# Kernel tuning notes

Measured on AMD Instinct MI355X. Metric: run time of the kernel, lower is better.

The kernel has to match this reference:

```python
import jax, jax.numpy as jnp
import numpy as np

N = 50000      # nodes
E = 600000     # edges
D_IN = 5
D_H = 128
EPS = 1e-5     # BatchNorm1d default eps


def batch_norm(x, gamma, beta):
    # training-mode BN over the node dimension (biased variance)
    m = jnp.mean(x, axis=0)
    v = jnp.var(x, axis=0)
    return (x - m) * jax.lax.rsqrt(v + EPS) * gamma + beta


def gcn_conv(x, W, b, src, dst, w):
    # PyG GCNConv: linear transform, add self-loops (weight 1),
    # symmetric normalization D^-1/2 A D^-1/2, scatter-add to dst, + bias.
    x = x @ W                                   # [N, out]
    n = x.shape[0]
    loop = jnp.arange(n)
    src = jnp.concatenate([src, loop])
    dst = jnp.concatenate([dst, loop])
    w = jnp.concatenate([w, jnp.ones((n,), w.dtype)])
    deg = jax.ops.segment_sum(w, dst, num_segments=n)
    dis = jnp.where(deg > 0, jax.lax.rsqrt(jnp.maximum(deg, 1e-12)), 0.0)
    norm = dis[src] * w * dis[dst]              # [E+N]
    msgs = norm[:, None] * x[src]               # gather + scale
    return jax.ops.segment_sum(msgs, dst, num_segments=n) + b


def setup_inputs() -> dict:
    key = jax.random.key(0)
    ks = jax.random.split(key, 20)
    s_in = 1.0 / np.sqrt(D_IN)
    s_h = 1.0 / np.sqrt(D_H)
    return {
        "h": jax.random.normal(ks[0], (N, D_IN), jnp.float32),
        "edge_index": jax.random.randint(ks[1], (2, E), 0, N),
        "edge_weight": jax.random.uniform(ks[2], (E,), jnp.float32),
        "g0": 1.0 + 0.1 * jax.random.normal(ks[3], (D_IN,), jnp.float32),
        "be0": 0.1 * jax.random.normal(ks[4], (D_IN,), jnp.float32),
        "W1": jax.random.normal(ks[5], (D_IN, D_H), jnp.float32) * s_in,
        "b1": jax.random.normal(ks[6], (D_H,), jnp.float32) * s_in,
        "g1": 1.0 + 0.1 * jax.random.normal(ks[7], (D_H,), jnp.float32),
        "be1": 0.1 * jax.random.normal(ks[8], (D_H,), jnp.float32),
        "W2": jax.random.normal(ks[9], (D_H, D_H), jnp.float32) * s_h,
        "b2": jax.random.normal(ks[10], (D_H,), jnp.float32) * s_h,
        "g2": 1.0 + 0.1 * jax.random.normal(ks[11], (D_H,), jnp.float32),
        "be2": 0.1 * jax.random.normal(ks[12], (D_H,), jnp.float32),
        "Wmu": jax.random.normal(ks[13], (D_H, D_H), jnp.float32) * s_h,
        "bmu": jax.random.normal(ks[14], (D_H,), jnp.float32) * s_h,
        "Wls": jax.random.normal(ks[15], (D_H, D_H), jnp.float32) * s_h,
        "bls": jax.random.normal(ks[16], (D_H,), jnp.float32) * s_h,
    }


def reference(h, edge_index, edge_weight, g0, be0, W1, b1, g1, be1,
              W2, b2, g2, be2, Wmu, bmu, Wls, bls):
    src, dst = edge_index[0], edge_index[1]
    h = batch_norm(h, g0, be0)
    h = jax.nn.relu(batch_norm(gcn_conv(h, W1, b1, src, dst, edge_weight), g1, be1))
    # dropout p=0.1 treated as eval-mode (identity)
    h = jax.nn.relu(batch_norm(gcn_conv(h, W2, b2, src, dst, edge_weight), g2, be2))
    mu = h @ Wmu + bmu
    log_std = h @ Wls + bls
    return (mu, log_std)
```

## Files before the change

### kernel.cpp

```cpp
#include <hip/hip_runtime.h>

#define N_NODES 50000
#define N_EDGES 600000
#define D_IN 5
#define D_H 128
#define BN_EPS 1e-5f
#define SCAN_BLOCKS ((N_NODES + 255) / 256)
#define DEG_BLOCKS ((N_EDGES + 255) / 256)
#define FIX_SCALE 16777216.0f
#define FIX_INV   (1.0f / 16777216.0f)

typedef __bf16 bf16x8 __attribute__((ext_vector_type(8)));
typedef float  f32x4  __attribute__((ext_vector_type(4)));

__device__ inline unsigned short f2bfb(float f) {
    unsigned u = __builtin_bit_cast(unsigned, f);
    unsigned r = u + 0x7fffu + ((u >> 16) & 1u);
    return (unsigned short)(r >> 16);
}
__device__ inline float bflo(unsigned u) { return __builtin_bit_cast(float, u << 16); }
__device__ inline float bfhi(unsigned u) { return __builtin_bit_cast(float, u & 0xffff0000u); }

__device__ inline void stage_b(const unsigned short* __restrict__ Bt,
                               uint4* __restrict__ lds, int t)
{
#pragma unroll
    for (int i = 0; i < 8; ++i) {
        int slot = i * 256 + t;
        int fid = slot >> 6;
        int l = slot & 63;
        int row = (fid >> 2) * 16 + (l & 15);
        int boff = ((l >> 4) * 16 + (fid & 3) * 64) >> 1;
        lds[slot] = *(const uint4*)(Bt + row * D_H + boff);
    }
}

__global__ __launch_bounds__(256) void k_prep(const float* __restrict__ W2,
                                              const float* __restrict__ Wmu,
                                              const float* __restrict__ Wls,
                                              unsigned short* __restrict__ T2,
                                              unsigned short* __restrict__ Tmu,
                                              unsigned short* __restrict__ Tls,
                                              const float* __restrict__ h,
                                              float* __restrict__ stats0,
                                              const int* __restrict__ dst,
                                              const float* __restrict__ w,
                                              unsigned long long* __restrict__ degcnt,
                                              int* __restrict__ rank)
{
    __shared__ float ss[D_IN], sq[D_IN];
    int b = blockIdx.x;
    int t = threadIdx.x;
    if (b < 192) {
        int mat = b >> 6;
        int idx = (b & 63) * 256 + t;
        const float* W = (mat == 0) ? W2 : (mat == 1) ? Wmu : Wls;
        unsigned short* T = (mat == 0) ? T2 : (mat == 1) ? Tmu : Tls;
        int k = idx >> 7, n = idx & 127;
        T[n * D_H + k] = f2bfb(W[idx]);
    } else if (b < 192 + SCAN_BLOCKS) {
        if (t < D_IN) { ss[t] = 0.f; sq[t] = 0.f; }
        __syncthreads();
        int node = (b - 192) * 256 + t;
        float v[D_IN];
#pragma unroll
        for (int f = 0; f < D_IN; ++f)
            v[f] = (node < N_NODES) ? h[node * D_IN + f] : 0.f;
        int lane = t & 63;
#pragma unroll
        for (int f = 0; f < D_IN; ++f) {
            float s = v[f], q = v[f] * v[f];
            for (int off = 32; off > 0; off >>= 1) {
                s += __shfl_down(s, off);
                q += __shfl_down(q, off);
            }
            if (lane == 0) { atomicAdd(&ss[f], s); atomicAdd(&sq[f], q); }
        }
        __syncthreads();
        if (t < D_IN) {
            atomicAdd(&stats0[t], ss[t]);
            atomicAdd(&stats0[D_IN + t], sq[t]);
        }
    } else {
        int e = (b - 192 - SCAN_BLOCKS) * 256 + t;
        if (e < N_EDGES) {
            int d = dst[e];
            unsigned long long fx = (unsigned long long)(w[e] * FIX_SCALE + 0.5f);
            unsigned long long old = atomicAdd(degcnt + d, (1ull << 40) | fx);
            rank[e] = (int)(old >> 40);
        }
    }
}

__global__ __launch_bounds__(256) void k_scan1(const unsigned long long* __restrict__ degcnt,
                                               float* __restrict__ dis,
                                               int* __restrict__ blocksums)
{
    __shared__ int sm[256];
    int t = threadIdx.x;
    int i = blockIdx.x * 256 + t;
    int c = 0;
    if (i < N_NODES) {
        unsigned long long v = degcnt[i];
        c = (int)(v >> 40);
        float deg = (float)(v & ((1ull << 40) - 1)) * FIX_INV;
        dis[i] = rsqrtf(deg + 1.0f);
    }
    sm[t] = c;
    __syncthreads();
    for (int off = 128; off > 0; off >>= 1) {
        if (t < off) sm[t] += sm[t + off];
        __syncthreads();
    }
    if (t == 0) blocksums[blockIdx.x] = sm[0];
}

__global__ __launch_bounds__(256) void k_scan3(const unsigned long long* __restrict__ degcnt,
                                               int* __restrict__ rowptr,
                                               const int* __restrict__ blocksums)
{
    __shared__ int bs[256];
    __shared__ int sm[256];
    int t = threadIdx.x;
    int bc = (t < SCAN_BLOCKS) ? blocksums[t] : 0;
    bs[t] = bc;
    __syncthreads();
    for (int off = 1; off < 256; off <<= 1) {
        int v = (t >= off) ? bs[t - off] : 0;
        __syncthreads();
        bs[t] += v;
        __syncthreads();
    }
    int prefix = (blockIdx.x == 0) ? 0 : bs[blockIdx.x - 1];
    if (blockIdx.x == SCAN_BLOCKS - 1 && t == 255)
        rowptr[N_NODES] = bs[SCAN_BLOCKS - 1];
    int i = blockIdx.x * 256 + t;
    int c = (i < N_NODES) ? (int)(degcnt[i] >> 40) : 0;
    sm[t] = c;
    __syncthreads();
    for (int off = 1; off < 256; off <<= 1) {
        int v = (t >= off) ? sm[t - off] : 0;
        __syncthreads();
        sm[t] += v;
        __syncthreads();
    }
    if (i < N_NODES)
        rowptr[i] = prefix + sm[t] - c;
}

__global__ __launch_bounds__(256) void k_fill(const int* __restrict__ src,
                                              const int* __restrict__ dst,
                                              const float* __restrict__ w,
                                              const float* __restrict__ dis,
                                              const int* __restrict__ rowptr,
                                              const int* __restrict__ rank,
                                              int2* __restrict__ csr)
{
    int e = blockIdx.x * blockDim.x + threadIdx.x;
    if (e < N_EDGES) {
        int s = src[e], d = dst[e];
        float pn = dis[s] * w[e];
        int pos = rowptr[d] + rank[e];
        int2 pk;
        pk.x = s;
        pk.y = __builtin_bit_cast(int, pn);
        csr[pos] = pk;
    }
}

__global__ __launch_bounds__(256) void k_agg0(const float* __restrict__ h,
                                              const float* __restrict__ stats,
                                              const float* __restrict__ g0,
                                              const float* __restrict__ be0,
                                              const int* __restrict__ rowptr,
                                              const int2* __restrict__ csr,
                                              const float* __restrict__ dis,
                                              float* __restrict__ agg)
{
    int n = blockIdx.x * blockDim.x + threadIdx.x;
    if (n >= N_NODES) return;
    float sc[D_IN], sh[D_IN];
#pragma unroll
    for (int f = 0; f < D_IN; ++f) {
        float m = stats[f] * (1.0f / N_NODES);
        float var = stats[D_IN + f] * (1.0f / N_NODES) - m * m;
        sc[f] = rsqrtf(var + BN_EPS) * g0[f];
        sh[f] = be0[f] - m * sc[f];
    }
    float dn = dis[n];
    float acc[D_IN];
#pragma unroll
    for (int f = 0; f < D_IN; ++f)
        acc[f] = dn * (h[n * D_IN + f] * sc[f] + sh[f]);
    int e0 = rowptr[n], e1 = rowptr[n + 1];
    for (int e = e0; e < e1; ++e) {
        int2 pk = csr[e];
        int s = pk.x;
        float pn = __builtin_bit_cast(float, pk.y);
#pragma unroll
        for (int f = 0; f < D_IN; ++f)
            acc[f] += pn * (h[s * D_IN + f] * sc[f] + sh[f]);
    }
#pragma unroll
    for (int f = 0; f < D_IN; ++f)
        agg[(size_t)n * 8 + f] = dn * acc[f];
}

__global__ __launch_bounds__(256) void k_l1(const float* __restrict__ agg,
                                            const float* __restrict__ W1,
                                            const float* __restrict__ b1,
                                            float* __restrict__ stats)
{
    __shared__ float sm_s[D_H], sm_q[D_H];
    int t = threadIdx.x;
    if (t < D_H) { sm_s[t] = 0.f; sm_q[t] = 0.f; }
    __syncthreads();
    int idx0 = blockIdx.x * 256 + t;
    int f0 = (idx0 & 63) * 2;
    float wa[D_IN], wb[D_IN];
#pragma unroll
    for (int k = 0; k < D_IN; ++k) {
        wa[k] = W1[k * D_H + f0];
        wb[k] = W1[k * D_H + f0 + 1];
    }
    float ba = b1[f0], bb = b1[f0 + 1];
    float s0 = 0.f, q0 = 0.f, s1 = 0.f, q1 = 0.f;
    const int stride = 512 * 256;
    for (int idx = idx0; idx < N_NODES * 64; idx += stride) {
        int n = idx >> 6;
        const float* a = agg + (size_t)n * 8;
        float v0 = ba, v1 = bb;
#pragma unroll
        for (int k = 0; k < D_IN; ++k) { v0 += wa[k] * a[k]; v1 += wb[k] * a[k]; }
        s0 += v0; q0 += v0 * v0; s1 += v1; q1 += v1 * v1;
    }
    atomicAdd(&sm_s[f0], s0); atomicAdd(&sm_s[f0 + 1], s1);
    atomicAdd(&sm_q[f0], q0); atomicAdd(&sm_q[f0 + 1], q1);
    __syncthreads();
    if (t < D_H) {
        atomicAdd(stats + t, sm_s[t]);
        atomicAdd(stats + D_H + t, sm_q[t]);
    }
}

__global__ __launch_bounds__(256) void k_agg_l1(const float* __restrict__ agg,
                                                const float* __restrict__ W1,
                                                const float* __restrict__ b1,
                                                const float* __restrict__ stats,
                                                const float* __restrict__ g,
                                                const float* __restrict__ be,
                                                const int* __restrict__ rowptr,
                                                const int2* __restrict__ csr,
                                                const float* __restrict__ dis,
                                                unsigned short* __restrict__ outb)
{
    int t = threadIdx.x;
    int n = blockIdx.x * 16 + (t >> 4);
    int f0 = (t & 15) * 8;
    if (n >= N_NODES) return;
    float wl[D_IN][8];
#pragma unroll
    for (int k = 0; k < D_IN; ++k) {
        float4 wlo = *(const float4*)(W1 + k * D_H + f0);
        float4 whi = *(const float4*)(W1 + k * D_H + f0 + 4);
        wl[k][0] = wlo.x; wl[k][1] = wlo.y; wl[k][2] = wlo.z; wl[k][3] = wlo.w;
        wl[k][4] = whi.x; wl[k][5] = whi.y; wl[k][6] = whi.z; wl[k][7] = whi.w;
    }
    float bv[8], sc[8], sh[8];
    const float inv = 1.0f / N_NODES;
#pragma unroll
    for (int j = 0; j < 8; ++j) {
        bv[j] = b1[f0 + j];
        float m = stats[f0 + j] * inv;
        float var = stats[D_H + f0 + j] * inv - m * m;
        sc[j] = rsqrtf(var + BN_EPS) * g[f0 + j];
        sh[j] = be[f0 + j] - m * sc[j];
    }
    float dn = dis[n];
    float acc[8];
    {
        float4 a03 = *(const float4*)(agg + (size_t)n * 8);
        float a4 = agg[(size_t)n * 8 + 4];
#pragma unroll
        for (int j = 0; j < 8; ++j) {
            float v = bv[j] + wl[0][j] * a03.x + wl[1][j] * a03.y
                    + wl[2][j] * a03.z + wl[3][j] * a03.w + wl[4][j] * a4;
            acc[j] = dn * fmaxf(v * sc[j] + sh[j], 0.f);
        }
    }
    int e = rowptr[n], e1 = rowptr[n + 1];
    for (; e + 2 <= e1; e += 2) {
        int2 p0 = csr[e], p1 = csr[e + 1];
        float w0 = __builtin_bit_cast(float, p0.y);
        float w1 = __builtin_bit_cast(float, p1.y);
        float4 x0 = *(const float4*)(agg + (size_t)p0.x * 8);
        float x04 = agg[(size_t)p0.x * 8 + 4];
        float4 x1 = *(const float4*)(agg + (size_t)p1.x * 8);
        float x14 = agg[(size_t)p1.x * 8 + 4];
#pragma unroll
        for (int j = 0; j < 8; ++j) {
            float v0 = bv[j] + wl[0][j] * x0.x + wl[1][j] * x0.y
                     + wl[2][j] * x0.z + wl[3][j] * x0.w + wl[4][j] * x04;
            float v1 = bv[j] + wl[0][j] * x1.x + wl[1][j] * x1.y
                     + wl[2][j] * x1.z + wl[3][j] * x1.w + wl[4][j] * x14;
            acc[j] += w0 * fmaxf(v0 * sc[j] + sh[j], 0.f)
                    + w1 * fmaxf(v1 * sc[j] + sh[j], 0.f);
        }
    }
    for (; e < e1; ++e) {
        int2 pk = csr[e];
        float pn = __builtin_bit_cast(float, pk.y);
        float4 x0 = *(const float4*)(agg + (size_t)pk.x * 8);
        float x04 = agg[(size_t)pk.x * 8 + 4];
#pragma unroll
        for (int j = 0; j < 8; ++j) {
            float v = bv[j] + wl[0][j] * x0.x + wl[1][j] * x0.y
                    + wl[2][j] * x0.z + wl[3][j] * x0.w + wl[4][j] * x04;
            acc[j] += pn * fmaxf(v * sc[j] + sh[j], 0.f);
        }
    }
    uint4 o;
    o.x = (unsigned)f2bfb(dn * acc[0]) | ((unsigned)f2bfb(dn * acc[1]) << 16);
    o.y = (unsigned)f2bfb(dn * acc[2]) | ((unsigned)f2bfb(dn * acc[3]) << 16);
    o.z = (unsigned)f2bfb(dn * acc[4]) | ((unsigned)f2bfb(dn * acc[5]) << 16);
    o.w = (unsigned)f2bfb(dn * acc[6]) | ((unsigned)f2bfb(dn * acc[7]) << 16);
    *(uint4*)(outb + (size_t)n * D_H + f0) = o;
}

__global__ __launch_bounds__(256) void k_gemm_mf(const unsigned short* __restrict__ A,
                                                 const unsigned short* __restrict__ Bt,
                                                 const float* __restrict__ bias,
                                                 unsigned short* __restrict__ C,
                                                 float* __restrict__ stats)
{
    __shared__ uint4 ldsB[2048];
    __shared__ float sm_s[D_H], sm_q[D_H];
    int t = threadIdx.x;
    if (t < D_H) { sm_s[t] = 0.f; sm_q[t] = 0.f; }
    stage_b(Bt, ldsB, t);
    int wave = t >> 6, lane = t & 63;
    int m = lane & 15, quad = lane >> 4;
    int r0 = blockIdx.x * 64 + wave * 16;
    int arow = r0 + m < N_NODES ? r0 + m : N_NODES - 1;
    const bf16x8* ap = (const bf16x8*)(A + (size_t)arow * D_H + quad * 8);
    bf16x8 af[4];
#pragma unroll
    for (int ks = 0; ks < 4; ++ks) af[ks] = ap[ks * 4];
    __syncthreads();
    const bf16x8* bf = (const bf16x8*)ldsB;
    f32x4 acc[8];
#pragma unroll
    for (int ct = 0; ct < 8; ++ct) acc[ct] = (f32x4)(0.f);
#pragma unroll
    for (int ks = 0; ks < 4; ++ks) {
#pragma unroll
        for (int ct = 0; ct < 8; ++ct) {
            acc[ct] = __builtin_amdgcn_mfma_f32_16x16x32_bf16(
                af[ks], bf[(ct * 4 + ks) * 64 + lane], acc[ct], 0, 0, 0);
        }
    }
#pragma unroll
    for (int ct = 0; ct < 8; ++ct) {
        int col = ct * 16 + m;
        float bvv = bias[col];
        float s = 0.f, q = 0.f;
#pragma unroll
        for (int r = 0; r < 4; ++r) {
            int rr = r0 + quad * 4 + r;
            if (rr < N_NODES) {
                float v = acc[ct][r] + bvv;
                C[(size_t)rr * D_H + col] = f2bfb(v);
                s += v; q += v * v;
            }
        }
        atomicAdd(&sm_s[col], s);
        atomicAdd(&sm_q[col], q);
    }
    __syncthreads();
    if (t < D_H) {
        atomicAdd(stats + t, sm_s[t]);
        atomicAdd(stats + D_H + t, sm_q[t]);
    }
}

__global__ __launch_bounds__(256) void k_gemm_out_mf(const unsigned short* __restrict__ A,
                                                     const float* __restrict__ stats,
                                                     const float* __restrict__ g,
                                                     const float* __restrict__ be,
                                                     const unsigned short* __restrict__ Btmu,
                                                     const float* __restrict__ bmu,
                                                     const unsigned short* __restrict__ Btls,
                                                     const float* __restrict__ bls,
                                                     float* __restrict__ out)
{
    __shared__ uint4 ldsB[2048];
    int t = threadIdx.x;
    int wave = t >> 6, lane = t & 63;
    int m = lane & 15, quad = lane >> 4;
    int r0 = blockIdx.x * 64 + wave * 16;
    int arow = r0 + m < N_NODES ? r0 + m : N_NODES - 1;
    const unsigned short* arowp = A + (size_t)arow * D_H + quad * 8;
    const float inv = 1.0f / N_NODES;
    bf16x8 af[4];
#pragma unroll
    for (int ks = 0; ks < 4; ++ks) {
        uint4 av = *(const uint4*)(arowp + ks * 32);
        float vals[8] = { bflo(av.x), bfhi(av.x), bflo(av.y), bfhi(av.y),
                          bflo(av.z), bfhi(av.z), bflo(av.w), bfhi(av.w) };
        int fb = quad * 8 + ks * 32;
        unsigned short o[8];
#pragma unroll
        for (int j = 0; j < 8; ++j) {
            int f = fb + j;
            float mm = stats[f] * inv;
            float var = stats[D_H + f] * inv - mm * mm;
            float scv = rsqrtf(var + BN_EPS) * g[f];
            float shv = be[f] - mm * scv;
            o[j] = f2bfb(fmaxf(vals[j] * scv + shv, 0.f));
        }
        uint4 pk;
        pk.x = (unsigned)o[0] | ((unsigned)o[1] << 16);
        pk.y = (unsigned)o[2] | ((unsigned)o[3] << 16);
        pk.z = (unsigned)o[4] | ((unsigned)o[5] << 16);
        pk.w = (unsigned)o[6] | ((unsigned)o[7] << 16);
        af[ks] = __builtin_bit_cast(bf16x8, pk);
    }
    const bf16x8* bf = (const bf16x8*)ldsB;
#pragma unroll
    for (int half = 0; half < 2; ++half) {
        if (half) __syncthreads();
        stage_b(half ? Btls : Btmu, ldsB, t);
        __syncthreads();
        const float* bias = half ? bls : bmu;
        float* C = out + (half ? (size_t)N_NODES * D_H : 0);
        f32x4 acc[8];
#pragma unroll
        for (int ct = 0; ct < 8; ++ct) acc[ct] = (f32x4)(0.f);
#pragma unroll
        for (int ks = 0; ks < 4; ++ks) {
#pragma unroll
            for (int ct = 0; ct < 8; ++ct) {
                acc[ct] = __builtin_amdgcn_mfma_f32_16x16x32_bf16(
                    af[ks], bf[(ct * 4 + ks) * 64 + lane], acc[ct], 0, 0, 0);
            }
        }
#pragma unroll
        for (int ct = 0; ct < 8; ++ct) {
            int col = ct * 16 + m;
            float bvv = bias[col];
#pragma unroll
            for (int r = 0; r < 4; ++r) {
                int rr = r0 + quad * 4 + r;
                if (rr < N_NODES)
                    C[(size_t)rr * D_H + col] = acc[ct][r] + bvv;
            }
        }
    }
}

extern "C" void kernel_launch(void* const* d_in, const int* in_sizes, int n_in,
                              void* d_out, int out_size, void* d_ws, size_t ws_size,
                              hipStream_t stream)
{
    const float* h   = (const float*)d_in[0];
    const int*   eidx = (const int*)d_in[1];
    const float* ew  = (const float*)d_in[2];
    const float* g0  = (const float*)d_in[3];
    const float* be0 = (const float*)d_in[4];
    const float* W1  = (const float*)d_in[5];
    const float* b1  = (const float*)d_in[6];
    const float* g1  = (const float*)d_in[7];
    const float* be1 = (const float*)d_in[8];
    const float* W2  = (const float*)d_in[9];
    const float* b2  = (const float*)d_in[10];
    const float* g2  = (const float*)d_in[11];
    const float* be2 = (const float*)d_in[12];
    const float* Wmu = (const float*)d_in[13];
    const float* bmu = (const float*)d_in[14];
    const float* Wls = (const float*)d_in[15];
    const float* bls = (const float*)d_in[16];
    const int* srcv = eidx;
    const int* dstv = eidx + N_EDGES;
    float* out = (float*)d_out;

    char* ws = (char*)d_ws;
    size_t off = 0;
    auto alloc = [&](size_t bytes) -> char* {
        char* p = ws + off;
        off += (bytes + 255) & ~(size_t)255;
        return p;
    };
    float* stats0  = (float*)alloc(16 * 4);
    float* stats1  = (float*)alloc(256 * 4);
    float* stats2  = (float*)alloc(256 * 4);
    unsigned long long* degcnt = (unsigned long long*)alloc(N_NODES * 8);
    size_t zero_bytes = off;
    int*   rowptr  = (int*)  alloc((N_NODES + 1) * 4);
    float* dis     = (float*)alloc(N_NODES * 4);
    int*   rank    = (int*)  alloc((size_t)N_EDGES * 4);
    int*   blocksums = (int*)alloc(256 * 4);
    int2*  csr     = (int2*) alloc((size_t)N_EDGES * 8);
    float* agg0    = (float*)alloc((size_t)N_NODES * 8 * 4);
    unsigned short* aggh = (unsigned short*)alloc((size_t)N_NODES * D_H * 2);
    unsigned short* c2h  = (unsigned short*)alloc((size_t)N_NODES * D_H * 2);
    unsigned short* Wt2   = (unsigned short*)alloc(D_H * D_H * 2);
    unsigned short* Wtmu  = (unsigned short*)alloc(D_H * D_H * 2);
    unsigned short* Wtls  = (unsigned short*)alloc(D_H * D_H * 2);
    (void)ws_size; (void)in_sizes; (void)n_in; (void)out_size;

    hipMemsetAsync(d_ws, 0, zero_bytes, stream);

    k_prep<<<192 + SCAN_BLOCKS + DEG_BLOCKS, 256, 0, stream>>>(
        W2, Wmu, Wls, Wt2, Wtmu, Wtls, h, stats0, dstv, ew, degcnt, rank);
    k_scan1<<<SCAN_BLOCKS, 256, 0, stream>>>(degcnt, dis, blocksums);
    k_scan3<<<SCAN_BLOCKS, 256, 0, stream>>>(degcnt, rowptr, blocksums);
    k_fill<<<DEG_BLOCKS, 256, 0, stream>>>(srcv, dstv, ew, dis, rowptr, rank, csr);
    k_agg0<<<SCAN_BLOCKS, 256, 0, stream>>>(h, stats0, g0, be0, rowptr, csr, dis, agg0);
    k_l1<<<512, 256, 0, stream>>>(agg0, W1, b1, stats1);
    k_agg_l1<<<(N_NODES + 15) / 16, 256, 0, stream>>>(agg0, W1, b1, stats1, g1, be1,
                                                      rowptr, csr, dis, aggh);
    k_gemm_mf<<<(N_NODES + 63) / 64, 256, 0, stream>>>(aggh, Wt2, b2, c2h, stats2);
    k_gemm_out_mf<<<(N_NODES + 63) / 64, 256, 0, stream>>>(c2h, stats2, g2, be2,
                                                           Wtmu, bmu, Wtls, bls, out);
}
```

Baseline: 301.1 us.

## Materialize layer-1 pre-BN features in bf16 and gather them in aggregation

k_l1 now writes the 128-wide layer-1 linear output as bf16 while computing BN stats, and the second aggregation kernel gathers these precomputed rows (one wave per node, two features per lane) instead of recomputing the 5x128 projection for every edge. This trades per-edge recomputation from compact 32-byte rows for gathers of 256-byte bf16 rows, plus an extra 12.8 MB write. It also adds bf16 rounding of the pre-BN activations.

```diff
diff --git a/kernel.cpp b/kernel.cpp
--- a/kernel.cpp
+++ b/kernel.cpp
@@ -209,6 +209,7 @@
 __global__ __launch_bounds__(256) void k_l1(const float* __restrict__ agg,
                                             const float* __restrict__ W1,
                                             const float* __restrict__ b1,
+                                            unsigned short* __restrict__ x,
                                             float* __restrict__ stats)
 {
     __shared__ float sm_s[D_H], sm_q[D_H];
@@ -232,6 +233,7 @@
         float v0 = ba, v1 = bb;
 #pragma unroll
         for (int k = 0; k < D_IN; ++k) { v0 += wa[k] * a[k]; v1 += wb[k] * a[k]; }
+        ((unsigned*)x)[idx] = (unsigned)f2bfb(v0) | ((unsigned)f2bfb(v1) << 16);
         s0 += v0; q0 += v0 * v0; s1 += v1; q1 += v1 * v1;
     }
     atomicAdd(&sm_s[f0], s0); atomicAdd(&sm_s[f0 + 1], s1);
@@ -243,9 +245,7 @@
     }
 }
 
-__global__ __launch_bounds__(256) void k_agg_l1(const float* __restrict__ agg,
-                                                const float* __restrict__ W1,
-                                                const float* __restrict__ b1,
+__global__ __launch_bounds__(256) void k_agg128(const unsigned short* __restrict__ x,
                                                 const float* __restrict__ stats,
                                                 const float* __restrict__ g,
                                                 const float* __restrict__ be,
@@ -255,76 +255,52 @@
                                                 unsigned short* __restrict__ outb)
 {
     int t = threadIdx.x;
-    int n = blockIdx.x * 16 + (t >> 4);
-    int f0 = (t & 15) * 8;
+    int n = blockIdx.x * 4 + (t >> 6);
+    int lane = t & 63;
+    int f0 = lane * 2;
     if (n >= N_NODES) return;
-    float wl[D_IN][8];
-#pragma unroll
-    for (int k = 0; k < D_IN; ++k) {
-        float4 wlo = *(const float4*)(W1 + k * D_H + f0);
-        float4 whi = *(const float4*)(W1 + k * D_H + f0 + 4);
-        wl[k][0] = wlo.x; wl[k][1] = wlo.y; wl[k][2] = wlo.z; wl[k][3] = wlo.w;
-        wl[k][4] = whi.x; wl[k][5] = whi.y; wl[k][6] = whi.z; wl[k][7] = whi.w;
-    }
-    float bv[8], sc[8], sh[8];
     const float inv = 1.0f / N_NODES;
-#pragma unroll
-    for (int j = 0; j < 8; ++j) {
-        bv[j] = b1[f0 + j];
-        float m = stats[f0 + j] * inv;
-        float var = stats[D_H + f0 + j] * inv - m * m;
-        sc[j] = rsqrtf(var + BN_EPS) * g[f0 + j];
-        sh[j] = be[f0 + j] - m * sc[j];
-    }
+    float m0 = stats[f0] * inv;
+    float v0v = stats[D_H + f0] * inv - m0 * m0;
+    float sc0 = rsqrtf(v0v + BN_EPS) * g[f0];
+    float sh0 = be[f0] - m0 * sc0;
+    float m1 = stats[f0 + 1] * inv;
+    float v1v = stats[D_H + f0 + 1] * inv - m1 * m1;
+    float sc1 = rsqrtf(v1v + BN_EPS) * g[f0 + 1];
+    float sh1 = be[f0 + 1] - m1 * sc1;
+#define BNR0(v) fmaxf((v) * sc0 + sh0, 0.f)
+#define BNR1(v) fmaxf((v) * sc1 + sh1, 0.f)
     float dn = dis[n];
-    float acc[8];
-    {
-        float4 a03 = *(const float4*)(agg + (size_t)n * 8);
-        float a4 = agg[(size_t)n * 8 + 4];
-#pragma unroll
-        for (int j = 0; j < 8; ++j) {
-            float v = bv[j] + wl[0][j] * a03.x + wl[1][j] * a03.y
-                    + wl[2][j] * a03.z + wl[3][j] * a03.w + wl[4][j] * a4;
-            acc[j] = dn * fmaxf(v * sc[j] + sh[j], 0.f);
-        }
-    }
+    unsigned hv = *(const unsigned*)(x + (size_t)n * D_H + f0);
+    float a0 = dn * BNR0(bflo(hv));
+    float a1 = dn * BNR1(bfhi(hv));
     int e = rowptr[n], e1 = rowptr[n + 1];
-    for (; e + 2 <= e1; e += 2) {
-        int2 p0 = csr[e], p1 = csr[e + 1];
+    for (; e + 4 <= e1; e += 4) {
+        int2 p0 = csr[e + 0], p1 = csr[e + 1], p2 = csr[e + 2], p3 = csr[e + 3];
         float w0 = __builtin_bit_cast(float, p0.y);
         float w1 = __builtin_bit_cast(float, p1.y);
-        float4 x0 = *(const float4*)(agg + (size_t)p0.x * 8);
-        float x04 = agg[(size_t)p0.x * 8 + 4];
-        float4 x1 = *(const float4*)(agg + (size_t)p1.x * 8);
-        float x14 = agg[(size_t)p1.x * 8 + 4];
-#pragma unroll
-        for (int j = 0; j < 8; ++j) {
-            float v0 = bv[j] + wl[0][j] * x0.x + wl[1][j] * x0.y
-                     + wl[2][j] * x0.z + wl[3][j] * x0.w + wl[4][j] * x04;
-            float v1 = bv[j] + wl[0][j] * x1.x + wl[1][j] * x1.y
-                     + wl[2][j] * x1.z + wl[3][j] * x1.w + wl[4][j] * x14;
-            acc[j] += w0 * fmaxf(v0 * sc[j] + sh[j], 0.f)
-                    + w1 * fmaxf(v1 * sc[j] + sh[j], 0.f);
-        }
+        float w2 = __builtin_bit_cast(float, p2.y);
+        float w3 = __builtin_bit_cast(float, p3.y);
+        unsigned v0 = *(const unsigned*)(x + (size_t)p0.x * D_H + f0);
+        unsigned v1 = *(const unsigned*)(x + (size_t)p1.x * D_H + f0);
+        unsigned v2 = *(const unsigned*)(x + (size_t)p2.x * D_H + f0);
+        unsigned v3 = *(const unsigned*)(x + (size_t)p3.x * D_H + f0);
+        a0 += w0 * BNR0(bflo(v0)) + w1 * BNR0(bflo(v1))
+            + w2 * BNR0(bflo(v2)) + w3 * BNR0(bflo(v3));
+        a1 += w0 * BNR1(bfhi(v0)) + w1 * BNR1(bfhi(v1))
+            + w2 * BNR1(bfhi(v2)) + w3 * BNR1(bfhi(v3));
     }
     for (; e < e1; ++e) {
         int2 pk = csr[e];
         float pn = __builtin_bit_cast(float, pk.y);
-        float4 x0 = *(const float4*)(agg + (size_t)pk.x * 8);
-        float x04 = agg[(size_t)pk.x * 8 + 4];
-#pragma unroll
-        for (int j = 0; j < 8; ++j) {
-            float v = bv[j] + wl[0][j] * x0.x + wl[1][j] * x0.y
-                    + wl[2][j] * x0.z + wl[3][j] * x0.w + wl[4][j] * x04;
-            acc[j] += pn * fmaxf(v * sc[j] + sh[j], 0.f);
-        }
-    }
-    uint4 o;
-    o.x = (unsigned)f2bfb(dn * acc[0]) | ((unsigned)f2bfb(dn * acc[1]) << 16);
-    o.y = (unsigned)f2bfb(dn * acc[2]) | ((unsigned)f2bfb(dn * acc[3]) << 16);
-    o.z = (unsigned)f2bfb(dn * acc[4]) | ((unsigned)f2bfb(dn * acc[5]) << 16);
-    o.w = (unsigned)f2bfb(dn * acc[6]) | ((unsigned)f2bfb(dn * acc[7]) << 16);
-    *(uint4*)(outb + (size_t)n * D_H + f0) = o;
+        unsigned v = *(const unsigned*)(x + (size_t)pk.x * D_H + f0);
+        a0 += pn * BNR0(bflo(v));
+        a1 += pn * BNR1(bfhi(v));
+    }
+#undef BNR0
+#undef BNR1
+    unsigned o = (unsigned)f2bfb(dn * a0) | ((unsigned)f2bfb(dn * a1) << 16);
+    *(unsigned*)(outb + (size_t)n * D_H + f0) = o;
 }
 
 __global__ __launch_bounds__(256) void k_gemm_mf(const unsigned short* __restrict__ A,
@@ -501,6 +477,7 @@
     int*   blocksums = (int*)alloc(256 * 4);
     int2*  csr     = (int2*) alloc((size_t)N_EDGES * 8);
     float* agg0    = (float*)alloc((size_t)N_NODES * 8 * 4);
+    unsigned short* x1h  = (unsigned short*)alloc((size_t)N_NODES * D_H * 2);
     unsigned short* aggh = (unsigned short*)alloc((size_t)N_NODES * D_H * 2);
     unsigned short* c2h  = (unsigned short*)alloc((size_t)N_NODES * D_H * 2);
     unsigned short* Wt2   = (unsigned short*)alloc(D_H * D_H * 2);
@@ -516,9 +493,9 @@
     k_scan3<<<SCAN_BLOCKS, 256, 0, stream>>>(degcnt, rowptr, blocksums);
     k_fill<<<DEG_BLOCKS, 256, 0, stream>>>(srcv, dstv, ew, dis, rowptr, rank, csr);
     k_agg0<<<SCAN_BLOCKS, 256, 0, stream>>>(h, stats0, g0, be0, rowptr, csr, dis, agg0);
-    k_l1<<<512, 256, 0, stream>>>(agg0, W1, b1, stats1);
-    k_agg_l1<<<(N_NODES + 15) / 16, 256, 0, stream>>>(agg0, W1, b1, stats1, g1, be1,
-                                                      rowptr, csr, dis, aggh);
+    k_l1<<<512, 256, 0, stream>>>(agg0, W1, b1, x1h, stats1);
+    k_agg128<<<(N_NODES + 3) / 4, 256, 0, stream>>>(x1h, stats1, g1, be1,
+                                                    rowptr, csr, dis, aggh);
     k_gemm_mf<<<(N_NODES + 63) / 64, 256, 0, stream>>>(aggh, Wt2, b2, c2h, stats2);
     k_gemm_out_mf<<<(N_NODES + 63) / 64, 256, 0, stream>>>(c2h, stats2, g2, be2,
                                                            Wtmu, bmu, Wtls, bls, out);
```

Result: faster. 287.9 us (-4.4%).
